# Kernel optimization log

Measured on AMD Instinct MI355X. Metric: run time of the kernel, lower is better.

## Reference

```python
import jax, jax.numpy as jnp
import numpy as np

N_NODES = 100000
N_EDGES = 1600000
IN_DIM, HID_DIM, OUT_DIM = 512, 128, 64


def setup_inputs() -> dict:
    key = jax.random.key(0)
    k1, k2, k3, k4, k5, k6 = jax.random.split(key, 6)
    feature = jax.random.normal(k1, (N_NODES, IN_DIM), dtype=jnp.float32)
    edge_row = jax.random.randint(k2, (N_EDGES,), 0, N_NODES, dtype=jnp.int32)
    edge_col = jax.random.randint(k3, (N_EDGES,), 0, N_NODES, dtype=jnp.int32)
    edge_vals = jax.random.uniform(k4, (N_EDGES,), dtype=jnp.float32)
    W1 = jax.random.normal(k5, (IN_DIM, HID_DIM), dtype=jnp.float32) * (IN_DIM ** -0.5)
    W2 = jax.random.normal(k6, (HID_DIM, OUT_DIM), dtype=jnp.float32) * (HID_DIM ** -0.5)
    return {"feature": feature, "edge_row": edge_row, "edge_col": edge_col,
            "edge_vals": edge_vals, "W1": W1, "W2": W2}


def spmm(edge_row, edge_col, edge_vals, dense):
    # sparse [N,N] @ dense [N,D]: out[r] += v * dense[c] for each edge (r,c,v)
    gathered = edge_vals[:, None] * dense[edge_col]  # [E, D]
    return jax.ops.segment_sum(gathered, edge_row, num_segments=N_NODES)


def reference(feature, edge_row, edge_col, edge_vals, W1, W2):
    # layer 1: support = X @ W1; h = relu(A @ support)
    h = jax.nn.relu(spmm(edge_row, edge_col, edge_vals, feature @ W1))
    # layer 2: logits = A @ (h @ W2)
    logits = spmm(edge_row, edge_col, edge_vals, h @ W2)
    return logits
```

## Files before the change

kernel.cpp:

```cpp
#include <hip/hip_runtime.h>

#define N_NODES 100000
#define N_EDGES 1600000
#define IN_DIM 512
#define HID_DIM 128
#define OUT_DIM 64

typedef __attribute__((ext_vector_type(8))) short bf16x8;
typedef __attribute__((ext_vector_type(4))) float f32x4;

__device__ __forceinline__ unsigned int f2bf_rne(float f) {
    union { float f; unsigned u; } v; v.f = f;
    unsigned r = v.u + 0x7fffu + ((v.u >> 16) & 1u);
    return r >> 16;
}

__global__ __launch_bounds__(256) void wcvt(const float* __restrict__ W1,
                                            unsigned short* __restrict__ W1t) {
    __shared__ float T[64][65];
    const int bk = blockIdx.x >> 1;
    const int bn = blockIdx.x & 1;
    const int t = threadIdx.x;
#pragma unroll
    for (int i = 0; i < 4; i++) {
        int fi = t + i * 256;
        int kk = fi >> 4;
        int f  = fi & 15;
        float4 v = *(const float4*)&W1[(long)(bk * 64 + kk) * HID_DIM + bn * 64 + f * 4];
        T[kk][f * 4 + 0] = v.x; T[kk][f * 4 + 1] = v.y;
        T[kk][f * 4 + 2] = v.z; T[kk][f * 4 + 3] = v.w;
    }
    __syncthreads();
#pragma unroll
    for (int i = 0; i < 8; i++) {
        int di = t + i * 256;
        int n  = di >> 5;
        int dw = di & 31;
        unsigned lo = f2bf_rne(T[dw * 2 + 0][n]);
        unsigned hi = f2bf_rne(T[dw * 2 + 1][n]);
        unsigned short* dst = W1t + (long)(bn * 64 + n) * IN_DIM + bk * 64 + dw * 2;
        *(unsigned int*)dst = lo | (hi << 16);
    }
}

__global__ __launch_bounds__(256) void wcvt2(const float* __restrict__ W2,
                                             unsigned short* __restrict__ W2t) {
    __shared__ float T[128][65];
    const int t = threadIdx.x;
#pragma unroll
    for (int i = 0; i < 8; i++) {
        int fi = t + i * 256;
        int k = fi >> 4;
        int f = fi & 15;
        float4 v = *(const float4*)&W2[(long)k * OUT_DIM + f * 4];
        T[k][f * 4 + 0] = v.x; T[k][f * 4 + 1] = v.y;
        T[k][f * 4 + 2] = v.z; T[k][f * 4 + 3] = v.w;
    }
    __syncthreads();
#pragma unroll
    for (int i = 0; i < 16; i++) {
        int di = t + i * 256;
        int n  = di >> 6;
        int dw = di & 63;
        unsigned lo = f2bf_rne(T[dw * 2 + 0][n]);
        unsigned hi = f2bf_rne(T[dw * 2 + 1][n]);
        *(unsigned int*)(W2t + (long)n * HID_DIM + dw * 2) = lo | (hi << 16);
    }
}

__global__ __launch_bounds__(256) void gemm1_mfma(const float* __restrict__ X,
                                                  const unsigned short* __restrict__ W1t,
                                                  unsigned short* __restrict__ outb) {
    __shared__ unsigned short As[64][40];
    const int tid  = threadIdx.x;
    const int lane = tid & 63;
    const int w    = tid >> 6;
    const int m    = lane & 15;
    const int hi   = lane >> 4;
    const int rowBase = blockIdx.x * 64;

    f32x4 acc[4][2] = {};

    const int sr = tid >> 2;
    const int sk = (tid & 3) * 8;
    int gr = rowBase + sr;
    if (gr >= N_NODES) gr = N_NODES - 1;
    const float* xp = X + (long)gr * IN_DIM;

    const unsigned short* b0p = W1t + (long)(w * 32 + m) * IN_DIM + hi * 8;
    const unsigned short* b1p = W1t + (long)(w * 32 + 16 + m) * IN_DIM + hi * 8;

    for (int k0 = 0; k0 < IN_DIM; k0 += 32) {
        float4 xa = *(const float4*)(xp + k0 + sk);
        float4 xb = *(const float4*)(xp + k0 + sk + 4);
        uint4 pk;
        pk.x = f2bf_rne(xa.x) | (f2bf_rne(xa.y) << 16);
        pk.y = f2bf_rne(xa.z) | (f2bf_rne(xa.w) << 16);
        pk.z = f2bf_rne(xb.x) | (f2bf_rne(xb.y) << 16);
        pk.w = f2bf_rne(xb.z) | (f2bf_rne(xb.w) << 16);
        *(uint4*)&As[sr][sk] = pk;
        __syncthreads();

        bf16x8 bf0 = *(const bf16x8*)(b0p + k0);
        bf16x8 bf1 = *(const bf16x8*)(b1p + k0);
#pragma unroll
        for (int t = 0; t < 4; t++) {
            bf16x8 af = *(const bf16x8*)&As[t * 16 + m][hi * 8];
            acc[t][0] = __builtin_amdgcn_mfma_f32_16x16x32_bf16(af, bf0, acc[t][0], 0, 0, 0);
            acc[t][1] = __builtin_amdgcn_mfma_f32_16x16x32_bf16(af, bf1, acc[t][1], 0, 0, 0);
        }
        __syncthreads();
    }

#pragma unroll
    for (int t = 0; t < 4; t++) {
#pragma unroll
        for (int r = 0; r < 4; r++) {
            int row = rowBase + t * 16 + hi * 4 + r;
            if (row < N_NODES) {
                outb[(long)row * HID_DIM + w * 32 + m] =
                    (unsigned short)f2bf_rne(acc[t][0][r]);
                outb[(long)row * HID_DIM + w * 32 + 16 + m] =
                    (unsigned short)f2bf_rne(acc[t][1][r]);
            }
        }
    }
}

__global__ __launch_bounds__(256) void gemm2_mfma(const unsigned short* __restrict__ hb,
                                                  const unsigned short* __restrict__ W2t,
                                                  unsigned short* __restrict__ hwb) {
    const int tid  = threadIdx.x;
    const int lane = tid & 63;
    const int w    = tid >> 6;
    const int m    = lane & 15;
    const int hi   = lane >> 4;
    const long rowBase = (long)blockIdx.x * 128 + w * 32;

    bf16x8 bfrag[4][4];
#pragma unroll
    for (int nt = 0; nt < 4; nt++) {
        const unsigned short* bp = W2t + (long)(nt * 16 + m) * HID_DIM + hi * 8;
#pragma unroll
        for (int ks = 0; ks < 4; ks++)
            bfrag[ks][nt] = *(const bf16x8*)(bp + ks * 32);
    }

    f32x4 acc[2][4] = {};
#pragma unroll
    for (int mt = 0; mt < 2; mt++) {
        long r = rowBase + mt * 16 + m;
        if (r >= N_NODES) r = N_NODES - 1;
        const unsigned short* ap = hb + r * HID_DIM + hi * 8;
#pragma unroll
        for (int ks = 0; ks < 4; ks++) {
            bf16x8 af = *(const bf16x8*)(ap + ks * 32);
#pragma unroll
            for (int nt = 0; nt < 4; nt++)
                acc[mt][nt] = __builtin_amdgcn_mfma_f32_16x16x32_bf16(
                    af, bfrag[ks][nt], acc[mt][nt], 0, 0, 0);
        }
    }

#pragma unroll
    for (int mt = 0; mt < 2; mt++)
#pragma unroll
        for (int nt = 0; nt < 4; nt++)
#pragma unroll
            for (int r = 0; r < 4; r++) {
                long row = rowBase + mt * 16 + hi * 4 + r;
                if (row < N_NODES)
                    hwb[row * OUT_DIM + nt * 16 + m] =
                        (unsigned short)f2bf_rne(acc[mt][nt][r]);
            }
}

#define ROWS_PER_GRP (N_NODES / 8)
#define CSR_BLOCKS 1024

__global__ __launch_bounds__(256) void hist_xcd(const int* __restrict__ rows,
                                                int* __restrict__ cnt) {
    const int grp = blockIdx.x & 7;
    const int rlo = grp * ROWS_PER_GRP;
    const int rhi = rlo + ROWS_PER_GRP;
    const int nb  = gridDim.x >> 3;
    const int bi  = blockIdx.x >> 3;
    for (int e = bi * 256 + threadIdx.x; e < N_EDGES; e += nb * 256) {
        int r = __builtin_nontemporal_load(&rows[e]);
        if (r >= rlo && r < rhi) atomicAdd(&cnt[r], 1);
    }
}

#define SCAN_BLOCKS ((N_NODES + 255) / 256)

__global__ __launch_bounds__(256) void scan_pass1(int* __restrict__ cnt,
                                                  int* __restrict__ bsum) {
    __shared__ int s[256];
    const int t = threadIdx.x;
    const int i = blockIdx.x * 256 + t;
    int v = (i < N_NODES) ? cnt[i] : 0;
    s[t] = v;
    __syncthreads();
    for (int off = 1; off < 256; off <<= 1) {
        int u = (t >= off) ? s[t - off] : 0;
        __syncthreads();
        s[t] += u;
        __syncthreads();
    }
    if (i < N_NODES) cnt[i] = s[t] - v;
    if (t == 255) bsum[blockIdx.x] = s[255];
}

__global__ __launch_bounds__(512) void scan_pass2(int* __restrict__ bsum,
                                                  int* __restrict__ boff) {
    __shared__ int s[512];
    const int t = threadIdx.x;
    int v = (t < SCAN_BLOCKS) ? bsum[t] : 0;
    s[t] = v;
    __syncthreads();
    for (int off = 1; off < 512; off <<= 1) {
        int u = (t >= off) ? s[t - off] : 0;
        __syncthreads();
        s[t] += u;
        __syncthreads();
    }
    if (t < SCAN_BLOCKS) boff[t] = s[t] - v;
}

__global__ __launch_bounds__(256) void scan_pass3(const int* __restrict__ cnt,
                                                  const int* __restrict__ boff,
                                                  int* __restrict__ rowptr,
                                                  int* __restrict__ cursor) {
    const int i = blockIdx.x * 256 + threadIdx.x;
    if (i < N_NODES) {
        int r = cnt[i] + boff[blockIdx.x];
        rowptr[i] = r;
        cursor[i] = r;
    }
    if (i == 0) rowptr[N_NODES] = N_EDGES;
}

__global__ __launch_bounds__(256) void scatter_xcd(const int* __restrict__ rows,
                                                   const int* __restrict__ cols,
                                                   const float* __restrict__ vals,
                                                   int* __restrict__ cursor,
                                                   int2* __restrict__ sedge) {
    const int grp = blockIdx.x & 7;
    const int rlo = grp * ROWS_PER_GRP;
    const int rhi = rlo + ROWS_PER_GRP;
    const int nb  = gridDim.x >> 3;
    const int bi  = blockIdx.x >> 3;
    for (int e = bi * 256 + threadIdx.x; e < N_EDGES; e += nb * 256) {
        int r = __builtin_nontemporal_load(&rows[e]);
        if (r >= rlo && r < rhi) {
            int   c = __builtin_nontemporal_load(&cols[e]);
            float v = __builtin_nontemporal_load(&vals[e]);
            int p = atomicAdd(&cursor[r], 1);
            sedge[p] = make_int2(c, __float_as_int(v));
        }
    }
}

__global__ __launch_bounds__(256) void spmm1(const int* __restrict__ rowptr,
                                             const int2* __restrict__ sedge,
                                             const unsigned short* __restrict__ supb,
                                             unsigned short* __restrict__ outb) {
    const int wid = blockIdx.x * 4 + (threadIdx.x >> 6);
    if (wid >= N_NODES) return;
    const int lane = threadIdx.x & 63;
    const int start = rowptr[wid];
    const int end   = rowptr[wid + 1];

    float accx = 0.f, accy = 0.f;

    for (int base = start; base < end; base += 64) {
        int idx = base + lane;
        int ecol = 0, eval = 0;
        if (idx < end) {
            int2 e = sedge[idx];
            ecol = e.x; eval = e.y;
        }
        const int cnt = min(64, end - base);
        for (int k = 0; k < cnt; k += 16) {
            int   c[16];
            float v[16];
#pragma unroll
            for (int q = 0; q < 16; q++) {
                c[q] = __builtin_amdgcn_readlane(ecol, k + q);
                v[q] = __int_as_float(__builtin_amdgcn_readlane(eval, k + q));
            }
            unsigned u[16];
#pragma unroll
            for (int q = 0; q < 16; q++)
                u[q] = *(const unsigned*)(supb + (long)c[q] * 128 + lane * 2);
#pragma unroll
            for (int q = 0; q < 16; q++) {
                accx += v[q] * __uint_as_float(u[q] << 16);
                accy += v[q] * __uint_as_float(u[q] & 0xffff0000u);
            }
        }
    }

    accx = accx > 0.f ? accx : 0.f;
    accy = accy > 0.f ? accy : 0.f;
    *(unsigned int*)(outb + (long)wid * 128 + lane * 2) =
        f2bf_rne(accx) | (f2bf_rne(accy) << 16);
}

__global__ __launch_bounds__(256) void spmm2(const int* __restrict__ rowptr,
                                             const int2* __restrict__ sedge,
                                             const unsigned short* __restrict__ hwb,
                                             float* __restrict__ out) {
    const int wid = blockIdx.x * 4 + (threadIdx.x >> 6);
    if (wid >= N_NODES) return;
    const int lane = threadIdx.x & 63;
    const int half = lane >> 5;
    const int hl   = lane & 31;
    const int start = rowptr[wid];
    const int end   = rowptr[wid + 1];

    float accx = 0.f, accy = 0.f;

    for (int base = start; base < end; base += 64) {
        int idx = base + lane;
        int ecol = 0, eval = 0;
        if (idx < end) {
            int2 e = sedge[idx];
            ecol = e.x; eval = e.y;
        }
        const int cnt = min(64, end - base);
        for (int k = 0; k < cnt; k += 16) {
            int   c[8];
            float v[8];
#pragma unroll
            for (int q = 0; q < 8; q++) {
                int c0 = __builtin_amdgcn_readlane(ecol, k + 2 * q);
                int c1 = __builtin_amdgcn_readlane(ecol, k + 2 * q + 1);
                int v0 = __builtin_amdgcn_readlane(eval, k + 2 * q);
                int v1 = __builtin_amdgcn_readlane(eval, k + 2 * q + 1);
                c[q] = half ? c1 : c0;
                v[q] = __int_as_float(half ? v1 : v0);
            }
            unsigned u[8];
#pragma unroll
            for (int q = 0; q < 8; q++)
                u[q] = *(const unsigned*)(hwb + (long)c[q] * OUT_DIM + hl * 2);
#pragma unroll
            for (int q = 0; q < 8; q++) {
                accx += v[q] * __uint_as_float(u[q] << 16);
                accy += v[q] * __uint_as_float(u[q] & 0xffff0000u);
            }
        }
    }

    accx += __shfl_xor(accx, 32);
    accy += __shfl_xor(accy, 32);
    if (half == 0) {
        float2 o = make_float2(accx, accy);
        *(float2*)(out + (long)wid * OUT_DIM + hl * 2) = o;
    }
}

extern "C" void kernel_launch(void* const* d_in, const int* in_sizes, int n_in,
                              void* d_out, int out_size, void* d_ws, size_t ws_size,
                              hipStream_t stream) {
    const float* feature = (const float*)d_in[0];
    const int*   erow    = (const int*)d_in[1];
    const int*   ecol    = (const int*)d_in[2];
    const float* evals   = (const float*)d_in[3];
    const float* W1      = (const float*)d_in[4];
    const float* W2      = (const float*)d_in[5];
    float* out = (float*)d_out;

    unsigned short* supb = (unsigned short*)d_ws;
    unsigned short* hb   = supb + (size_t)N_NODES * HID_DIM;
    unsigned short* hwb  = hb + (size_t)N_NODES * HID_DIM;
    int*   cnt     = (int*)(hwb + (size_t)N_NODES * OUT_DIM);
    int*   cursor  = cnt + N_NODES;
    int*   rowptr  = cursor + N_NODES;
    int2*  sedge   = (int2*)(rowptr + (N_NODES + 2));
    int*   bsum    = (int*)(sedge + N_EDGES);
    int*   boff    = bsum + SCAN_BLOCKS;
    unsigned short* W1t = (unsigned short*)(boff + SCAN_BLOCKS);
    unsigned short* W2t = W1t + (size_t)HID_DIM * IN_DIM;

    hipMemsetAsync(cnt, 0, (size_t)N_NODES * sizeof(int), stream);
    hist_xcd<<<CSR_BLOCKS, 256, 0, stream>>>(erow, cnt);
    scan_pass1<<<SCAN_BLOCKS, 256, 0, stream>>>(cnt, bsum);
    scan_pass2<<<1, 512, 0, stream>>>(bsum, boff);
    scan_pass3<<<SCAN_BLOCKS, 256, 0, stream>>>(cnt, boff, rowptr, cursor);
    scatter_xcd<<<CSR_BLOCKS, 256, 0, stream>>>(erow, ecol, evals, cursor, sedge);

    wcvt<<<16, 256, 0, stream>>>(W1, W1t);
    wcvt2<<<1, 256, 0, stream>>>(W2, W2t);

    gemm1_mfma<<<(N_NODES + 63) / 64, 256, 0, stream>>>(feature, W1t, supb);

    spmm1<<<(N_NODES + 3) / 4, 256, 0, stream>>>(rowptr, sedge, supb, hb);

    gemm2_mfma<<<(N_NODES + 127) / 128, 256, 0, stream>>>(hb, W2t, hwb);

    spmm2<<<(N_NODES + 3) / 4, 256, 0, stream>>>(rowptr, sedge, hwb, out);
}
```

Baseline: 602.6 us.

## Restructure gemm1 to per-wave row tiles without LDS and merge weight conversion kernels

gemm1 no longer stages X through shared memory with two barriers per k-step. Each wave now owns 16 rows and all 128 output columns, loading its A fragment straight from global memory into registers and reading W1t fragments directly, so the __syncthreads calls go away. The two weight-conversion kernels are merged into one launch to save a kernel launch. In exchange each wave loads 8 B fragments per k-step instead of 2 and keeps more accumulators in registers, and the X reads are less coalesced per lane.

```diff
diff --git a/kernel.cpp b/kernel.cpp
--- a/kernel.cpp
+++ b/kernel.cpp
@@ -15,114 +15,100 @@
     return r >> 16;
 }
 
-__global__ __launch_bounds__(256) void wcvt(const float* __restrict__ W1,
-                                            unsigned short* __restrict__ W1t) {
-    __shared__ float T[64][65];
-    const int bk = blockIdx.x >> 1;
-    const int bn = blockIdx.x & 1;
-    const int t = threadIdx.x;
-#pragma unroll
-    for (int i = 0; i < 4; i++) {
-        int fi = t + i * 256;
-        int kk = fi >> 4;
-        int f  = fi & 15;
-        float4 v = *(const float4*)&W1[(long)(bk * 64 + kk) * HID_DIM + bn * 64 + f * 4];
-        T[kk][f * 4 + 0] = v.x; T[kk][f * 4 + 1] = v.y;
-        T[kk][f * 4 + 2] = v.z; T[kk][f * 4 + 3] = v.w;
-    }
-    __syncthreads();
-#pragma unroll
-    for (int i = 0; i < 8; i++) {
-        int di = t + i * 256;
-        int n  = di >> 5;
-        int dw = di & 31;
-        unsigned lo = f2bf_rne(T[dw * 2 + 0][n]);
-        unsigned hi = f2bf_rne(T[dw * 2 + 1][n]);
-        unsigned short* dst = W1t + (long)(bn * 64 + n) * IN_DIM + bk * 64 + dw * 2;
-        *(unsigned int*)dst = lo | (hi << 16);
-    }
-}
-
-__global__ __launch_bounds__(256) void wcvt2(const float* __restrict__ W2,
-                                             unsigned short* __restrict__ W2t) {
+__global__ __launch_bounds__(256) void wcvt_all(const float* __restrict__ W1,
+                                                unsigned short* __restrict__ W1t,
+                                                const float* __restrict__ W2,
+                                                unsigned short* __restrict__ W2t) {
     __shared__ float T[128][65];
     const int t = threadIdx.x;
-#pragma unroll
-    for (int i = 0; i < 8; i++) {
-        int fi = t + i * 256;
-        int k = fi >> 4;
-        int f = fi & 15;
-        float4 v = *(const float4*)&W2[(long)k * OUT_DIM + f * 4];
-        T[k][f * 4 + 0] = v.x; T[k][f * 4 + 1] = v.y;
-        T[k][f * 4 + 2] = v.z; T[k][f * 4 + 3] = v.w;
-    }
-    __syncthreads();
-#pragma unroll
-    for (int i = 0; i < 16; i++) {
-        int di = t + i * 256;
-        int n  = di >> 6;
-        int dw = di & 63;
-        unsigned lo = f2bf_rne(T[dw * 2 + 0][n]);
-        unsigned hi = f2bf_rne(T[dw * 2 + 1][n]);
-        *(unsigned int*)(W2t + (long)n * HID_DIM + dw * 2) = lo | (hi << 16);
+    if (blockIdx.x < 16) {
+        const int bk = blockIdx.x >> 1;
+        const int bn = blockIdx.x & 1;
+#pragma unroll
+        for (int i = 0; i < 4; i++) {
+            int fi = t + i * 256;
+            int kk = fi >> 4;
+            int f  = fi & 15;
+            float4 v = *(const float4*)&W1[(long)(bk * 64 + kk) * HID_DIM + bn * 64 + f * 4];
+            T[kk][f * 4 + 0] = v.x; T[kk][f * 4 + 1] = v.y;
+            T[kk][f * 4 + 2] = v.z; T[kk][f * 4 + 3] = v.w;
+        }
+        __syncthreads();
+#pragma unroll
+        for (int i = 0; i < 8; i++) {
+            int di = t + i * 256;
+            int n  = di >> 5;
+            int dw = di & 31;
+            unsigned lo = f2bf_rne(T[dw * 2 + 0][n]);
+            unsigned hi = f2bf_rne(T[dw * 2 + 1][n]);
+            unsigned short* dst = W1t + (long)(bn * 64 + n) * IN_DIM + bk * 64 + dw * 2;
+            *(unsigned int*)dst = lo | (hi << 16);
+        }
+    } else {
+#pragma unroll
+        for (int i = 0; i < 8; i++) {
+            int fi = t + i * 256;
+            int k = fi >> 4;
+            int f = fi & 15;
+            float4 v = *(const float4*)&W2[(long)k * OUT_DIM + f * 4];
+            T[k][f * 4 + 0] = v.x; T[k][f * 4 + 1] = v.y;
+            T[k][f * 4 + 2] = v.z; T[k][f * 4 + 3] = v.w;
+        }
+        __syncthreads();
+#pragma unroll
+        for (int i = 0; i < 16; i++) {
+            int di = t + i * 256;
+            int n  = di >> 6;
+            int dw = di & 63;
+            unsigned lo = f2bf_rne(T[dw * 2 + 0][n]);
+            unsigned hi = f2bf_rne(T[dw * 2 + 1][n]);
+            *(unsigned int*)(W2t + (long)n * HID_DIM + dw * 2) = lo | (hi << 16);
+        }
     }
 }
 
 __global__ __launch_bounds__(256) void gemm1_mfma(const float* __restrict__ X,
                                                   const unsigned short* __restrict__ W1t,
                                                   unsigned short* __restrict__ outb) {
-    __shared__ unsigned short As[64][40];
     const int tid  = threadIdx.x;
     const int lane = tid & 63;
     const int w    = tid >> 6;
     const int m    = lane & 15;
     const int hi   = lane >> 4;
-    const int rowBase = blockIdx.x * 64;
-
-    f32x4 acc[4][2] = {};
-
-    const int sr = tid >> 2;
-    const int sk = (tid & 3) * 8;
-    int gr = rowBase + sr;
+    const int rowBase = blockIdx.x * 64 + w * 16;
+
+    int gr = rowBase + m;
     if (gr >= N_NODES) gr = N_NODES - 1;
-    const float* xp = X + (long)gr * IN_DIM;
-
-    const unsigned short* b0p = W1t + (long)(w * 32 + m) * IN_DIM + hi * 8;
-    const unsigned short* b1p = W1t + (long)(w * 32 + 16 + m) * IN_DIM + hi * 8;
-
+    const float* xp = X + (long)gr * IN_DIM + hi * 8;
+
+    const unsigned short* bp = W1t + (long)m * IN_DIM + hi * 8;
+
+    f32x4 acc[8] = {};
+
+#pragma unroll 4
     for (int k0 = 0; k0 < IN_DIM; k0 += 32) {
-        float4 xa = *(const float4*)(xp + k0 + sk);
-        float4 xb = *(const float4*)(xp + k0 + sk + 4);
-        uint4 pk;
-        pk.x = f2bf_rne(xa.x) | (f2bf_rne(xa.y) << 16);
-        pk.y = f2bf_rne(xa.z) | (f2bf_rne(xa.w) << 16);
-        pk.z = f2bf_rne(xb.x) | (f2bf_rne(xb.y) << 16);
-        pk.w = f2bf_rne(xb.z) | (f2bf_rne(xb.w) << 16);
-        *(uint4*)&As[sr][sk] = pk;
-        __syncthreads();
-
-        bf16x8 bf0 = *(const bf16x8*)(b0p + k0);
-        bf16x8 bf1 = *(const bf16x8*)(b1p + k0);
-#pragma unroll
-        for (int t = 0; t < 4; t++) {
-            bf16x8 af = *(const bf16x8*)&As[t * 16 + m][hi * 8];
-            acc[t][0] = __builtin_amdgcn_mfma_f32_16x16x32_bf16(af, bf0, acc[t][0], 0, 0, 0);
-            acc[t][1] = __builtin_amdgcn_mfma_f32_16x16x32_bf16(af, bf1, acc[t][1], 0, 0, 0);
-        }
-        __syncthreads();
-    }
-
-#pragma unroll
-    for (int t = 0; t < 4; t++) {
+        float4 xa = *(const float4*)(xp + k0);
+        float4 xb = *(const float4*)(xp + k0 + 4);
+        union { unsigned u[4]; bf16x8 v; } af;
+        af.u[0] = f2bf_rne(xa.x) | (f2bf_rne(xa.y) << 16);
+        af.u[1] = f2bf_rne(xa.z) | (f2bf_rne(xa.w) << 16);
+        af.u[2] = f2bf_rne(xb.x) | (f2bf_rne(xb.y) << 16);
+        af.u[3] = f2bf_rne(xb.z) | (f2bf_rne(xb.w) << 16);
+#pragma unroll
+        for (int nt = 0; nt < 8; nt++) {
+            bf16x8 bf = *(const bf16x8*)(bp + (long)nt * 16 * IN_DIM + k0);
+            acc[nt] = __builtin_amdgcn_mfma_f32_16x16x32_bf16(af.v, bf, acc[nt], 0, 0, 0);
+        }
+    }
+
+#pragma unroll
+    for (int nt = 0; nt < 8; nt++) {
 #pragma unroll
         for (int r = 0; r < 4; r++) {
-            int row = rowBase + t * 16 + hi * 4 + r;
-            if (row < N_NODES) {
-                outb[(long)row * HID_DIM + w * 32 + m] =
-                    (unsigned short)f2bf_rne(acc[t][0][r]);
-                outb[(long)row * HID_DIM + w * 32 + 16 + m] =
-                    (unsigned short)f2bf_rne(acc[t][1][r]);
-            }
+            int row = rowBase + hi * 4 + r;
+            if (row < N_NODES)
+                outb[(long)row * HID_DIM + nt * 16 + m] =
+                    (unsigned short)f2bf_rne(acc[nt][r]);
         }
     }
 }
@@ -391,8 +377,7 @@
     scan_pass3<<<SCAN_BLOCKS, 256, 0, stream>>>(cnt, boff, rowptr, cursor);
     scatter_xcd<<<CSR_BLOCKS, 256, 0, stream>>>(erow, ecol, evals, cursor, sedge);
 
-    wcvt<<<16, 256, 0, stream>>>(W1, W1t);
-    wcvt2<<<1, 256, 0, stream>>>(W2, W2t);
+    wcvt_all<<<17, 256, 0, stream>>>(W1, W1t, W2, W2t);
 
     gemm1_mfma<<<(N_NODES + 63) / 64, 256, 0, stream>>>(feature, W1t, supb);
 
```

After: 661.8 us. 9.8% more time.
